# Kernel optimization log

Measured on AMD Instinct MI355X. Metric: run time of the kernel, lower is better.

## Reference

```python
import jax, jax.numpy as jnp
import numpy as np

B, S, E, H = 2, 2048, 1024, 16
DH = E // H  # 64


def setup_inputs() -> dict:
    key = jax.random.key(0)
    ks = jax.random.split(key, 10)
    scale = 1.0 / np.sqrt(E)
    x = jax.random.normal(ks[0], (B, S, E), dtype=jnp.float32)
    mask = jax.random.randint(ks[1], (B, S), 0, 2, dtype=jnp.int32)
    # per-head Q/K/V projections stacked: [H, E, DH] (x @ W, torch Linear transposed)
    wq = jax.random.normal(ks[2], (H, E, DH), dtype=jnp.float32) * scale
    wk = jax.random.normal(ks[3], (H, E, DH), dtype=jnp.float32) * scale
    wv = jax.random.normal(ks[4], (H, E, DH), dtype=jnp.float32) * scale
    bq = jax.random.normal(ks[5], (H, DH), dtype=jnp.float32) * scale
    bk = jax.random.normal(ks[6], (H, DH), dtype=jnp.float32) * scale
    bv = jax.random.normal(ks[7], (H, DH), dtype=jnp.float32) * scale
    wo = jax.random.normal(ks[8], (E, E), dtype=jnp.float32) * scale
    bo = jax.random.normal(ks[9], (E,), dtype=jnp.float32) * scale
    return {"x": x, "mask": mask, "wq": wq, "bq": bq, "wk": wk, "bk": bk,
            "wv": wv, "bv": bv, "wo": wo, "bo": bo}


def reference(x, mask, wq, bq, wk, bk, wv, bv, wo, bo):
    # q,k,v: [B, H, S, DH]
    q = jnp.einsum('bse,hed->bhsd', x, wq) + bq[None, :, None, :]
    k = jnp.einsum('bse,hed->bhsd', x, wk) + bk[None, :, None, :]
    v = jnp.einsum('bse,hed->bhsd', x, wv) + bv[None, :, None, :]
    scores = jnp.einsum('bhsd,bhtd->bhst', q, k) / np.sqrt(DH)
    # padding mask on key axis: mask==0 -> -1e9 (as in masked_fill)
    scores = jnp.where(mask[:, None, None, :] == 0, jnp.float32(-1e9), scores)
    attn = jax.nn.softmax(scores, axis=-1)
    o = jnp.einsum('bhst,bhtd->bhsd', attn, v)
    # concat heads -> [B, S, E], then output projection
    o = o.transpose(0, 2, 1, 3).reshape(B, S, E)
    return o @ wo + bo
```

## Files before the change

### kernel.cpp

```cpp
#include <hip/hip_runtime.h>
#include <hip/hip_bf16.h>
#include <math.h>

#define Bsz 2
#define Ssz 2048
#define Esz 1024
#define Hsz 16
#define DHsz 64

typedef __bf16 bf16_t;
typedef __attribute__((ext_vector_type(8))) __bf16 bf16x8;
typedef __attribute__((ext_vector_type(4))) float f32x4;

typedef unsigned int u32;
typedef const __attribute__((address_space(1))) u32* gptr_t;
typedef __attribute__((address_space(3))) u32* lptr_t;

#if __has_builtin(__builtin_amdgcn_exp2f)
#define EXP2F(x) __builtin_amdgcn_exp2f(x)
#else
#define EXP2F(x) __expf((x)*0.69314718f)
#endif

__device__ __forceinline__ bf16_t to_bf16(float f) {
  union { float f; unsigned u; } v; v.f = f;
  unsigned r = (v.u + 0x7FFF + ((v.u >> 16) & 1)) >> 16;
  union { unsigned short s; bf16_t b; } o; o.s = (unsigned short)r;
  return o.b;
}

__device__ __forceinline__ unsigned pack2(float a, float b) {
  union { float f; unsigned u; } x, y; x.f = a; y.f = b;
  unsigned ra = (x.u + 0x7FFF + ((x.u >> 16) & 1)) >> 16;
  unsigned rb = (y.u + 0x7FFF + ((y.u >> 16) & 1)) >> 16;
  return ra | (rb << 16);
}

__device__ __forceinline__ f32x4 mfma16(bf16x8 a, bf16x8 b, f32x4 c) {
  return __builtin_amdgcn_mfma_f32_16x16x32_bf16(a, b, c, 0, 0, 0);
}

__device__ __forceinline__ void gload16(void* lds, const void* g) {
  __builtin_amdgcn_global_load_lds((gptr_t)g, (lptr_t)lds, 16, 0, 0);
}

__global__ void cast_x4(const float4* __restrict__ x, uint2* __restrict__ xb, int n4) {
  int i = blockIdx.x * blockDim.x + threadIdx.x;
  if (i < n4) {
    float4 v = x[i];
    uint2 o; o.x = pack2(v.x, v.y); o.y = pack2(v.z, v.w);
    xb[i] = o;
  }
}

__global__ void mask_f(const int* __restrict__ mask, float* __restrict__ mf, int n) {
  int i = blockIdx.x * blockDim.x + threadIdx.x;
  if (i < n) mf[i] = mask[i] ? 1.0f : 0.0f;
}

__global__ __launch_bounds__(256) void wtrans(
    const float* __restrict__ wq, const float* __restrict__ wk,
    const float* __restrict__ wv, const float* __restrict__ wo,
    bf16_t* __restrict__ wAll, bf16_t* __restrict__ wAllV, bf16_t* __restrict__ woT) {
  __shared__ bf16_t lT[64 * 72];
  const int et = blockIdx.x, h = blockIdx.y, z = blockIdx.z;
  const float* src; int srcLD; bf16_t* dst;
  if (z == 0)      { src = wq + ((size_t)h * Esz + et * 64) * DHsz; srcLD = DHsz; dst = wAll  + (size_t)(h * 64) * Esz; }
  else if (z == 1) { src = wk + ((size_t)h * Esz + et * 64) * DHsz; srcLD = DHsz; dst = wAll  + (size_t)(1024 + h * 64) * Esz; }
  else if (z == 2) { src = wv + ((size_t)h * Esz + et * 64) * DHsz; srcLD = DHsz; dst = wAllV + (size_t)(h * 64) * Esz; }
  else             { src = wo + (size_t)(et * 64) * Esz + h * 64;   srcLD = Esz;  dst = woT   + (size_t)(h * 64) * Esz; }
  const int t = threadIdx.x;
#pragma unroll
  for (int rr = 0; rr < 4; rr++) {
    int er = rr * 16 + (t >> 4);
    int dc = (t & 15) * 4;
    float4 v = *(const float4*)&src[(size_t)er * srcLD + dc];
    lT[(dc + 0) * 72 + er] = to_bf16(v.x);
    lT[(dc + 1) * 72 + er] = to_bf16(v.y);
    lT[(dc + 2) * 72 + er] = to_bf16(v.z);
    lT[(dc + 3) * 72 + er] = to_bf16(v.w);
  }
  __syncthreads();
#pragma unroll
  for (int rr = 0; rr < 2; rr++) {
    int d = rr * 32 + (t >> 3);
    int e8 = (t & 7) * 8;
    bf16x8 o = *(const bf16x8*)&lT[d * 72 + e8];
    *(bf16x8*)&dst[(size_t)d * Esz + et * 64 + e8] = o;
  }
}

template <int TM, int TN>
__device__ __forceinline__ void gemm_core(
    const bf16_t* __restrict__ Ab, const bf16_t* __restrict__ Bb, int K,
    bf16_t* lA, bf16_t* lB, f32x4 (&acc)[TM / 32][TN / 32]) {
  const int tid = threadIdx.x, lane = tid & 63, wvi = tid >> 6;
  const int g = lane >> 4, c = lane & 15, cw = c & 7;
  const int lrow = lane >> 3, sg = lane & 7;
  const int wm = wvi >> 1, wn = wvi & 1;
  for (int kc = 0; kc < K; kc += 64) {
#pragma unroll
    for (int j = 0; j < TM / 32; j++) {
      const int base = (j * 4 + wvi) * 8;
      const int row = base + lrow;
      gload16(lA + base * 64, Ab + (size_t)row * K + kc + ((sg ^ (row & 7)) * 8));
    }
#pragma unroll
    for (int j = 0; j < TN / 32; j++) {
      const int base = (j * 4 + wvi) * 8;
      const int row = base + lrow;
      gload16(lB + base * 64, Bb + (size_t)row * K + kc + ((sg ^ (row & 7)) * 8));
    }
    __syncthreads();
#pragma unroll
    for (int ksp = 0; ksp < 2; ksp++) {
      const int kg = (ksp * 4 + g) ^ cw;
      bf16x8 af[TM / 32], bfr[TN / 32];
#pragma unroll
      for (int mt = 0; mt < TM / 32; mt++)
        af[mt] = *(const bf16x8*)&lA[(wm * (TM / 2) + mt * 16 + c) * 64 + kg * 8];
#pragma unroll
      for (int nt = 0; nt < TN / 32; nt++)
        bfr[nt] = *(const bf16x8*)&lB[(wn * (TN / 2) + nt * 16 + c) * 64 + kg * 8];
#pragma unroll
      for (int mt = 0; mt < TM / 32; mt++)
#pragma unroll
        for (int nt = 0; nt < TN / 32; nt++)
          acc[mt][nt] = mfma16(af[mt], bfr[nt], acc[mt][nt]);
    }
    __syncthreads();
  }
}

__global__ __launch_bounds__(256, 2) void qk_gemm(
    const bf16_t* __restrict__ xb, const bf16_t* __restrict__ wAll,
    const float* __restrict__ bq, const float* __restrict__ bk,
    bf16_t* __restrict__ qb, bf16_t* __restrict__ kb) {
  __shared__ alignas(16) bf16_t lA[128 * 64];
  __shared__ alignas(16) bf16_t lB[128 * 64];
  f32x4 acc[4][4] = {};
  const int Mb = blockIdx.x * 128, Nb = blockIdx.y * 128;
  gemm_core<128, 128>(xb + (size_t)Mb * Esz, wAll + (size_t)Nb * Esz, Esz, lA, lB, acc);
  const int lane = threadIdx.x & 63, wvi = threadIdx.x >> 6;
  const int g = lane >> 4, c = lane & 15;
  const int wm = wvi >> 1, wn = wvi & 1;
#pragma unroll
  for (int nt = 0; nt < 4; nt++) {
    const int col = Nb + wn * 64 + nt * 16 + c;
    const int which = col >> 10, h = (col >> 6) & 15, d = col & 63;
    const float bias = (which ? bk : bq)[h * DHsz + d];
    const float scale = which ? 1.0f : 0.18033688011112042f;
    bf16_t* dst = which ? kb : qb;
#pragma unroll
    for (int mt = 0; mt < 4; mt++)
#pragma unroll
      for (int r = 0; r < 4; r++) {
        const int row = Mb + wm * 64 + mt * 16 + g * 4 + r;
        const int b = row >> 11, s = row & 2047;
        dst[(((size_t)(b * Hsz + h)) * Ssz + s) * DHsz + d] =
            to_bf16((acc[mt][nt][r] + bias) * scale);
      }
  }
}

__global__ __launch_bounds__(256, 2) void vt_gemm(
    const bf16_t* __restrict__ xb, const bf16_t* __restrict__ wAllV,
    const float* __restrict__ bv, bf16_t* __restrict__ vTb) {
  __shared__ alignas(16) bf16_t lA[64 * 64];
  __shared__ alignas(16) bf16_t lB[128 * 64];
  f32x4 acc[2][4] = {};
  const int Mb = blockIdx.x * 64, Nb = blockIdx.y * 128, b = blockIdx.z;
  gemm_core<64, 128>(wAllV + (size_t)Mb * Esz, xb + ((size_t)(b * Ssz) + Nb) * Esz,
                     Esz, lA, lB, acc);
  const int lane = threadIdx.x & 63, wvi = threadIdx.x >> 6;
  const int g = lane >> 4, c = lane & 15;
  const int wm = wvi >> 1, wn = wvi & 1;
#pragma unroll
  for (int mt = 0; mt < 2; mt++)
#pragma unroll
    for (int r = 0; r < 4; r++) {
      const int m = Mb + wm * 32 + mt * 16 + g * 4 + r;
      const float bias = bv[m];
      const size_t obase = ((size_t)(b * Hsz * DHsz + m)) * Ssz;
#pragma unroll
      for (int nt = 0; nt < 4; nt++) {
        const int s = Nb + wn * 64 + nt * 16 + c;
        vTb[obase + s] = to_bf16(acc[mt][nt][r] + bias);
      }
    }
}

__global__ __launch_bounds__(256, 3) void flash_attn(
    const bf16_t* __restrict__ qb, const bf16_t* __restrict__ kb,
    const bf16_t* __restrict__ vTb, const float* __restrict__ mf,
    bf16_t* __restrict__ Ob) {
  __shared__ alignas(16) bf16_t lK0[64 * 64];
  __shared__ alignas(16) bf16_t lV0[64 * 64];
  __shared__ alignas(16) bf16_t lK1[64 * 64];
  __shared__ alignas(16) bf16_t lV1[64 * 64];
  __shared__ alignas(16) bf16_t lP[4][32 * 64];
  __shared__ float lL[4][32];

  const int h = blockIdx.x, qt = blockIdx.y, b = blockIdx.z;
  const size_t bh = (size_t)(b * Hsz + h);
  const int tid = threadIdx.x, lane = tid & 63, wv = tid >> 6;
  const int g = lane >> 4, c = lane & 15, cw = c & 7;
  const int lrow = lane >> 3, sg = lane & 7;

  const bf16_t* Kbase = kb + bh * (size_t)Ssz * DHsz;
  const bf16_t* Vbase = vTb + bh * (size_t)DHsz * Ssz;
  const float* mbase = mf + b * Ssz;

  bf16x8 qf[2][2];
  const bf16_t* Qbase = qb + (bh * Ssz + qt * 128 + wv * 32) * DHsz;
#pragma unroll
  for (int qsub = 0; qsub < 2; qsub++)
#pragma unroll
    for (int ksp = 0; ksp < 2; ksp++)
      qf[qsub][ksp] = *(const bf16x8*)&Qbase[(qsub * 16 + c) * DHsz + ksp * 32 + g * 8];

  f32x4 o[2][4] = {};
  float lacc[2] = {0.f, 0.f};

  auto stage = [&](bf16_t* dK, bf16_t* dV, int tc) {
#pragma unroll
    for (int j = 0; j < 2; j++) {
      const int row = wv * 16 + j * 8 + lrow;
      const int kg = sg ^ (row & 7);
      gload16(dK + (wv * 16 + j * 8) * 64,
              Kbase + ((size_t)(tc * 64 + row)) * DHsz + kg * 8);
      gload16(dV + (wv * 16 + j * 8) * 64,
              Vbase + (size_t)row * Ssz + tc * 64 + kg * 8);
    }
  };

  auto compute = [&](const bf16_t* Kt, const bf16_t* Vt, int tc) {
    f32x4 st[2][4] = {};
#pragma unroll
    for (int ksp = 0; ksp < 2; ksp++) {
      const int kgr = (ksp * 4 + g) ^ cw;
#pragma unroll
      for (int nt = 0; nt < 4; nt++) {
        bf16x8 kf = *(const bf16x8*)&Kt[(nt * 16 + c) * 64 + kgr * 8];
        st[0][nt] = mfma16(kf, qf[0][ksp], st[0][nt]);
        st[1][nt] = mfma16(kf, qf[1][ksp], st[1][nt]);
      }
    }
    float4 mv[4];
#pragma unroll
    for (int nt = 0; nt < 4; nt++)
      mv[nt] = *(const float4*)&mbase[tc * 64 + nt * 16 + g * 4];
#pragma unroll
    for (int qsub = 0; qsub < 2; qsub++) {
      float part = 0.f;
#pragma unroll
      for (int nt = 0; nt < 4; nt++) {
        float p0 = EXP2F(st[qsub][nt][0]) * mv[nt].x;
        float p1 = EXP2F(st[qsub][nt][1]) * mv[nt].y;
        float p2 = EXP2F(st[qsub][nt][2]) * mv[nt].z;
        float p3 = EXP2F(st[qsub][nt][3]) * mv[nt].w;
        part += (p0 + p1) + (p2 + p3);
        const int pg = (nt * 2 + (g >> 1)) ^ cw;
        uint2 pv; pv.x = pack2(p0, p1); pv.y = pack2(p2, p3);
        *(uint2*)&lP[wv][(qsub * 16 + c) * 64 + pg * 8 + (g & 1) * 4] = pv;
      }
      lacc[qsub] += part;
    }
#pragma unroll
    for (int ksp = 0; ksp < 2; ksp++) {
      const int kgr = (ksp * 4 + g) ^ cw;
      bf16x8 pf0 = *(const bf16x8*)&lP[wv][(0 * 16 + c) * 64 + kgr * 8];
      bf16x8 pf1 = *(const bf16x8*)&lP[wv][(1 * 16 + c) * 64 + kgr * 8];
#pragma unroll
      for (int dt = 0; dt < 4; dt++) {
        bf16x8 vf = *(const bf16x8*)&Vt[(dt * 16 + c) * 64 + kgr * 8];
        o[0][dt] = mfma16(pf0, vf, o[0][dt]);
        o[1][dt] = mfma16(pf1, vf, o[1][dt]);
      }
    }
  };

  stage(lK0, lV0, 0);
  __syncthreads();
  for (int tc = 0; tc < 32; tc += 2) {
    stage(lK1, lV1, tc + 1);
    compute(lK0, lV0, tc);
    __syncthreads();
    if (tc + 2 < 32) stage(lK0, lV0, tc + 2);
    compute(lK1, lV1, tc + 1);
    __syncthreads();
  }

#pragma unroll
  for (int qsub = 0; qsub < 2; qsub++) {
    float v = lacc[qsub];
    v += __shfl_xor(v, 16);
    v += __shfl_xor(v, 32);
    lL[wv][qsub * 16 + c] = v;
  }
#pragma unroll
  for (int qsub = 0; qsub < 2; qsub++)
#pragma unroll
    for (int r = 0; r < 4; r++) {
      const int row = qsub * 16 + g * 4 + r;
      const float linv = 1.0f / fmaxf(lL[wv][row], 1e-30f);
      const size_t orow = (size_t)(b * Ssz + qt * 128 + wv * 32 + row) * Esz + h * DHsz;
#pragma unroll
      for (int dt = 0; dt < 4; dt++)
        Ob[orow + dt * 16 + c] = to_bf16(o[qsub][dt][r] * linv);
    }
}

__global__ __launch_bounds__(256, 2) void out_gemm(
    const bf16_t* __restrict__ Ob, const bf16_t* __restrict__ woT,
    const float* __restrict__ bo, float* __restrict__ out) {
  __shared__ alignas(16) bf16_t lA[128 * 64];
  __shared__ alignas(16) bf16_t lB[64 * 64];
  f32x4 acc[4][2] = {};
  const int Mb = blockIdx.x * 128, Nb = blockIdx.y * 64;
  gemm_core<128, 64>(Ob + (size_t)Mb * Esz, woT + (size_t)Nb * Esz, Esz, lA, lB, acc);
  const int lane = threadIdx.x & 63, wvi = threadIdx.x >> 6;
  const int g = lane >> 4, c = lane & 15;
  const int wm = wvi >> 1, wn = wvi & 1;
#pragma unroll
  for (int nt = 0; nt < 2; nt++) {
    const int col = Nb + wn * 32 + nt * 16 + c;
    const float bias = bo[col];
#pragma unroll
    for (int mt = 0; mt < 4; mt++)
#pragma unroll
      for (int r = 0; r < 4; r++) {
        const int row = Mb + wm * 64 + mt * 16 + g * 4 + r;
        out[(size_t)row * Esz + col] = acc[mt][nt][r] + bias;
      }
  }
}

extern "C" void kernel_launch(void* const* d_in, const int* in_sizes, int n_in,
                              void* d_out, int out_size, void* d_ws, size_t ws_size,
                              hipStream_t stream) {
  const float* x = (const float*)d_in[0];
  const int* mask = (const int*)d_in[1];
  const float* wq = (const float*)d_in[2];
  const float* bq = (const float*)d_in[3];
  const float* wk = (const float*)d_in[4];
  const float* bk = (const float*)d_in[5];
  const float* wv = (const float*)d_in[6];
  const float* bv = (const float*)d_in[7];
  const float* wo = (const float*)d_in[8];
  const float* bo = (const float*)d_in[9];
  float* out = (float*)d_out;

  char* ws = (char*)d_ws;
  size_t off = 0;
  auto take = [&](size_t bytes) -> char* {
    char* p = ws + off;
    off += (bytes + 255) & ~(size_t)255;
    return p;
  };
  bf16_t* xb    = (bf16_t*)take((size_t)Bsz * Ssz * Esz * 2);
  bf16_t* wAll  = (bf16_t*)take((size_t)2 * Esz * Esz * 2);
  bf16_t* wAllV = (bf16_t*)take((size_t)Esz * Esz * 2);
  bf16_t* woT   = (bf16_t*)take((size_t)Esz * Esz * 2);
  bf16_t* qb    = (bf16_t*)take((size_t)Bsz * Hsz * Ssz * DHsz * 2);
  bf16_t* kb    = (bf16_t*)take((size_t)Bsz * Hsz * Ssz * DHsz * 2);
  bf16_t* vTb   = (bf16_t*)take((size_t)Bsz * Hsz * Ssz * DHsz * 2);
  bf16_t* Ob    = (bf16_t*)take((size_t)Bsz * Ssz * Esz * 2);
  float*  mfp   = (float*)take((size_t)Bsz * Ssz * 4);

  const int n4 = Bsz * Ssz * Esz / 4;
  cast_x4<<<(n4 + 255) / 256, 256, 0, stream>>>((const float4*)x, (uint2*)xb, n4);
  mask_f<<<(Bsz * Ssz + 255) / 256, 256, 0, stream>>>(mask, mfp, Bsz * Ssz);
  wtrans<<<dim3(Esz / 64, Hsz, 4), 256, 0, stream>>>(wq, wk, wv, wo, wAll, wAllV, woT);

  qk_gemm<<<dim3(Bsz * Ssz / 128, 2 * Esz / 128), 256, 0, stream>>>(xb, wAll, bq, bk, qb, kb);
  vt_gemm<<<dim3(Esz / 64, Ssz / 128, Bsz), 256, 0, stream>>>(xb, wAllV, bv, vTb);
  flash_attn<<<dim3(Hsz, Ssz / 128, Bsz), 256, 0, stream>>>(qb, kb, vTb, mfp, Ob);
  out_gemm<<<dim3(Bsz * Ssz / 128, Esz / 64), 256, 0, stream>>>(Ob, woT, bo, out);
}
```

Baseline: 212.8 us.

## Fuse prep and QKV launches, fold mask into V, load K/V directly to registers

```diff
diff --git a/kernel.cpp b/kernel.cpp
--- a/kernel.cpp
+++ b/kernel.cpp
@@ -29,6 +29,14 @@
   return o.b;
 }
 
+__device__ __forceinline__ unsigned pack2_rtz(float a, float b) {
+#if __has_builtin(__builtin_amdgcn_perm)
+  return __builtin_amdgcn_perm(__float_as_uint(b), __float_as_uint(a), 0x07060302u);
+#else
+  return (__float_as_uint(a) >> 16) | (__float_as_uint(b) & 0xFFFF0000u);
+#endif
+}
+
 __device__ __forceinline__ unsigned pack2(float a, float b) {
   union { float f; unsigned u; } x, y; x.f = a; y.f = b;
   unsigned ra = (x.u + 0x7FFF + ((x.u >> 16) & 1)) >> 16;
@@ -44,49 +52,50 @@
   __builtin_amdgcn_global_load_lds((gptr_t)g, (lptr_t)lds, 16, 0, 0);
 }
 
-__global__ void cast_x4(const float4* __restrict__ x, uint2* __restrict__ xb, int n4) {
-  int i = blockIdx.x * blockDim.x + threadIdx.x;
-  if (i < n4) {
-    float4 v = x[i];
-    uint2 o; o.x = pack2(v.x, v.y); o.y = pack2(v.z, v.w);
-    xb[i] = o;
-  }
-}
-
-__global__ void mask_f(const int* __restrict__ mask, float* __restrict__ mf, int n) {
-  int i = blockIdx.x * blockDim.x + threadIdx.x;
-  if (i < n) mf[i] = mask[i] ? 1.0f : 0.0f;
-}
-
-__global__ __launch_bounds__(256) void wtrans(
+#define PREP_CAST 4096
+#define PREP_MASK 4112
+__global__ __launch_bounds__(256) void prep(
+    const float* __restrict__ x, const int* __restrict__ mask,
     const float* __restrict__ wq, const float* __restrict__ wk,
     const float* __restrict__ wv, const float* __restrict__ wo,
+    bf16_t* __restrict__ xb, bf16_t* __restrict__ mb,
     bf16_t* __restrict__ wAll, bf16_t* __restrict__ wAllV, bf16_t* __restrict__ woT) {
   __shared__ bf16_t lT[64 * 72];
-  const int et = blockIdx.x, h = blockIdx.y, z = blockIdx.z;
-  const float* src; int srcLD; bf16_t* dst;
-  if (z == 0)      { src = wq + ((size_t)h * Esz + et * 64) * DHsz; srcLD = DHsz; dst = wAll  + (size_t)(h * 64) * Esz; }
-  else if (z == 1) { src = wk + ((size_t)h * Esz + et * 64) * DHsz; srcLD = DHsz; dst = wAll  + (size_t)(1024 + h * 64) * Esz; }
-  else if (z == 2) { src = wv + ((size_t)h * Esz + et * 64) * DHsz; srcLD = DHsz; dst = wAllV + (size_t)(h * 64) * Esz; }
-  else             { src = wo + (size_t)(et * 64) * Esz + h * 64;   srcLD = Esz;  dst = woT   + (size_t)(h * 64) * Esz; }
-  const int t = threadIdx.x;
-#pragma unroll
-  for (int rr = 0; rr < 4; rr++) {
-    int er = rr * 16 + (t >> 4);
-    int dc = (t & 15) * 4;
-    float4 v = *(const float4*)&src[(size_t)er * srcLD + dc];
-    lT[(dc + 0) * 72 + er] = to_bf16(v.x);
-    lT[(dc + 1) * 72 + er] = to_bf16(v.y);
-    lT[(dc + 2) * 72 + er] = to_bf16(v.z);
-    lT[(dc + 3) * 72 + er] = to_bf16(v.w);
-  }
-  __syncthreads();
-#pragma unroll
-  for (int rr = 0; rr < 2; rr++) {
-    int d = rr * 32 + (t >> 3);
-    int e8 = (t & 7) * 8;
-    bf16x8 o = *(const bf16x8*)&lT[d * 72 + e8];
-    *(bf16x8*)&dst[(size_t)d * Esz + et * 64 + e8] = o;
+  const int bid = blockIdx.x, t = threadIdx.x;
+  if (bid < PREP_CAST) {
+    const int i = bid * 256 + t;
+    float4 v = ((const float4*)x)[i];
+    uint2 o; o.x = pack2(v.x, v.y); o.y = pack2(v.z, v.w);
+    ((uint2*)xb)[i] = o;
+  } else if (bid < PREP_MASK) {
+    const int i = (bid - PREP_CAST) * 256 + t;
+    mb[i] = to_bf16(mask[i] ? 1.0f : 0.0f);
+  } else {
+    const int t2 = bid - PREP_MASK;
+    const int et = t2 & 15, h = (t2 >> 4) & 15, z = t2 >> 8;
+    const float* src; int srcLD; bf16_t* dst;
+    if (z == 0)      { src = wq + ((size_t)h * Esz + et * 64) * DHsz; srcLD = DHsz; dst = wAll  + (size_t)(h * 64) * Esz; }
+    else if (z == 1) { src = wk + ((size_t)h * Esz + et * 64) * DHsz; srcLD = DHsz; dst = wAll  + (size_t)(1024 + h * 64) * Esz; }
+    else if (z == 2) { src = wv + ((size_t)h * Esz + et * 64) * DHsz; srcLD = DHsz; dst = wAllV + (size_t)(h * 64) * Esz; }
+    else             { src = wo + (size_t)(et * 64) * Esz + h * 64;   srcLD = Esz;  dst = woT   + (size_t)(h * 64) * Esz; }
+#pragma unroll
+    for (int rr = 0; rr < 4; rr++) {
+      int er = rr * 16 + (t >> 4);
+      int dc = (t & 15) * 4;
+      float4 v = *(const float4*)&src[(size_t)er * srcLD + dc];
+      lT[(dc + 0) * 72 + er] = to_bf16(v.x);
+      lT[(dc + 1) * 72 + er] = to_bf16(v.y);
+      lT[(dc + 2) * 72 + er] = to_bf16(v.z);
+      lT[(dc + 3) * 72 + er] = to_bf16(v.w);
+    }
+    __syncthreads();
+#pragma unroll
+    for (int rr = 0; rr < 2; rr++) {
+      int d = rr * 32 + (t >> 3);
+      int e8 = (t & 7) * 8;
+      bf16x8 o = *(const bf16x8*)&lT[d * 72 + e8];
+      *(bf16x8*)&dst[(size_t)d * Esz + et * 64 + e8] = o;
+    }
   }
 }
 
@@ -132,84 +141,75 @@
   }
 }
 
-__global__ __launch_bounds__(256, 2) void qk_gemm(
+__global__ __launch_bounds__(256, 2) void qkv_gemm(
     const bf16_t* __restrict__ xb, const bf16_t* __restrict__ wAll,
+    const bf16_t* __restrict__ wAllV, const bf16_t* __restrict__ mb,
     const float* __restrict__ bq, const float* __restrict__ bk,
-    bf16_t* __restrict__ qb, bf16_t* __restrict__ kb) {
+    const float* __restrict__ bv,
+    bf16_t* __restrict__ qb, bf16_t* __restrict__ kb, bf16_t* __restrict__ vTb) {
   __shared__ alignas(16) bf16_t lA[128 * 64];
   __shared__ alignas(16) bf16_t lB[128 * 64];
-  f32x4 acc[4][4] = {};
-  const int Mb = blockIdx.x * 128, Nb = blockIdx.y * 128;
-  gemm_core<128, 128>(xb + (size_t)Mb * Esz, wAll + (size_t)Nb * Esz, Esz, lA, lB, acc);
+  const int bid = blockIdx.x;
   const int lane = threadIdx.x & 63, wvi = threadIdx.x >> 6;
   const int g = lane >> 4, c = lane & 15;
   const int wm = wvi >> 1, wn = wvi & 1;
-#pragma unroll
-  for (int nt = 0; nt < 4; nt++) {
-    const int col = Nb + wn * 64 + nt * 16 + c;
-    const int which = col >> 10, h = (col >> 6) & 15, d = col & 63;
-    const float bias = (which ? bk : bq)[h * DHsz + d];
-    const float scale = which ? 1.0f : 0.18033688011112042f;
-    bf16_t* dst = which ? kb : qb;
-#pragma unroll
-    for (int mt = 0; mt < 4; mt++)
-#pragma unroll
-      for (int r = 0; r < 4; r++) {
-        const int row = Mb + wm * 64 + mt * 16 + g * 4 + r;
-        const int b = row >> 11, s = row & 2047;
-        dst[(((size_t)(b * Hsz + h)) * Ssz + s) * DHsz + d] =
-            to_bf16((acc[mt][nt][r] + bias) * scale);
-      }
-  }
-}
-
-__global__ __launch_bounds__(256, 2) void vt_gemm(
-    const bf16_t* __restrict__ xb, const bf16_t* __restrict__ wAllV,
-    const float* __restrict__ bv, bf16_t* __restrict__ vTb) {
-  __shared__ alignas(16) bf16_t lA[64 * 64];
-  __shared__ alignas(16) bf16_t lB[128 * 64];
-  f32x4 acc[2][4] = {};
-  const int Mb = blockIdx.x * 64, Nb = blockIdx.y * 128, b = blockIdx.z;
-  gemm_core<64, 128>(wAllV + (size_t)Mb * Esz, xb + ((size_t)(b * Ssz) + Nb) * Esz,
-                     Esz, lA, lB, acc);
-  const int lane = threadIdx.x & 63, wvi = threadIdx.x >> 6;
-  const int g = lane >> 4, c = lane & 15;
-  const int wm = wvi >> 1, wn = wvi & 1;
-#pragma unroll
-  for (int mt = 0; mt < 2; mt++)
-#pragma unroll
-    for (int r = 0; r < 4; r++) {
-      const int m = Mb + wm * 32 + mt * 16 + g * 4 + r;
-      const float bias = bv[m];
-      const size_t obase = ((size_t)(b * Hsz * DHsz + m)) * Ssz;
-#pragma unroll
-      for (int nt = 0; nt < 4; nt++) {
-        const int s = Nb + wn * 64 + nt * 16 + c;
-        vTb[obase + s] = to_bf16(acc[mt][nt][r] + bias);
-      }
-    }
-}
-
-__global__ __launch_bounds__(256, 3) void flash_attn(
+  if (bid < 512) {
+    f32x4 acc[4][4] = {};
+    const int Mb = (bid & 31) * 128, Nb = (bid >> 5) * 128;
+    gemm_core<128, 128>(xb + (size_t)Mb * Esz, wAll + (size_t)Nb * Esz, Esz, lA, lB, acc);
+#pragma unroll
+    for (int nt = 0; nt < 4; nt++) {
+      const int col = Nb + wn * 64 + nt * 16 + c;
+      const int which = col >> 10, h = (col >> 6) & 15, d = col & 63;
+      const float bias = (which ? bk : bq)[h * DHsz + d];
+      const float scale = which ? 1.0f : 0.18033688011112042f;
+      bf16_t* dst = which ? kb : qb;
+#pragma unroll
+      for (int mt = 0; mt < 4; mt++)
+#pragma unroll
+        for (int r = 0; r < 4; r++) {
+          const int row = Mb + wm * 64 + mt * 16 + g * 4 + r;
+          const int b = row >> 11, s = row & 2047;
+          dst[(((size_t)(b * Hsz + h)) * Ssz + s) * DHsz + d] =
+              to_bf16((acc[mt][nt][r] + bias) * scale);
+        }
+    }
+  } else {
+    const int t2 = bid - 512;
+    f32x4 acc[2][4] = {};
+    const int Mb = (t2 & 15) * 64, Nb = ((t2 >> 4) & 15) * 128, b = t2 >> 8;
+    gemm_core<64, 128>(wAllV + (size_t)Mb * Esz, xb + ((size_t)(b * Ssz) + Nb) * Esz,
+                       Esz, lA, lB, acc);
+#pragma unroll
+    for (int nt = 0; nt < 4; nt++) {
+      const int s = Nb + wn * 64 + nt * 16 + c;
+      const float mval = (float)mb[b * Ssz + s];
+#pragma unroll
+      for (int mt = 0; mt < 2; mt++)
+#pragma unroll
+        for (int r = 0; r < 4; r++) {
+          const int m = Mb + wm * 32 + mt * 16 + g * 4 + r;
+          const size_t obase = ((size_t)(b * Hsz * DHsz + m)) * Ssz;
+          vTb[obase + s] = to_bf16((acc[mt][nt][r] + bv[m]) * mval);
+        }
+    }
+  }
+}
+
+__global__ __launch_bounds__(256, 2) void flash_attn(
     const bf16_t* __restrict__ qb, const bf16_t* __restrict__ kb,
-    const bf16_t* __restrict__ vTb, const float* __restrict__ mf,
+    const bf16_t* __restrict__ vTb, const bf16_t* __restrict__ mb,
     bf16_t* __restrict__ Ob) {
-  __shared__ alignas(16) bf16_t lK0[64 * 64];
-  __shared__ alignas(16) bf16_t lV0[64 * 64];
-  __shared__ alignas(16) bf16_t lK1[64 * 64];
-  __shared__ alignas(16) bf16_t lV1[64 * 64];
   __shared__ alignas(16) bf16_t lP[4][32 * 64];
-  __shared__ float lL[4][32];
 
   const int h = blockIdx.x, qt = blockIdx.y, b = blockIdx.z;
   const size_t bh = (size_t)(b * Hsz + h);
   const int tid = threadIdx.x, lane = tid & 63, wv = tid >> 6;
   const int g = lane >> 4, c = lane & 15, cw = c & 7;
-  const int lrow = lane >> 3, sg = lane & 7;
-
-  const bf16_t* Kbase = kb + bh * (size_t)Ssz * DHsz;
-  const bf16_t* Vbase = vTb + bh * (size_t)DHsz * Ssz;
-  const float* mbase = mf + b * Ssz;
+
+  const bf16_t* Kbase = kb + bh * (size_t)Ssz * DHsz + c * DHsz + g * 8;
+  const bf16_t* Vbase = vTb + bh * (size_t)DHsz * Ssz + c * Ssz + g * 8;
+  const bf16_t* mbb = mb + b * Ssz + g * 8;
 
   bf16x8 qf[2][2];
   const bf16_t* Qbase = qb + (bh * Ssz + qt * 128 + wv * 32) * DHsz;
@@ -220,90 +220,76 @@
       qf[qsub][ksp] = *(const bf16x8*)&Qbase[(qsub * 16 + c) * DHsz + ksp * 32 + g * 8];
 
   f32x4 o[2][4] = {};
-  float lacc[2] = {0.f, 0.f};
-
-  auto stage = [&](bf16_t* dK, bf16_t* dV, int tc) {
-#pragma unroll
-    for (int j = 0; j < 2; j++) {
-      const int row = wv * 16 + j * 8 + lrow;
-      const int kg = sg ^ (row & 7);
-      gload16(dK + (wv * 16 + j * 8) * 64,
-              Kbase + ((size_t)(tc * 64 + row)) * DHsz + kg * 8);
-      gload16(dV + (wv * 16 + j * 8) * 64,
-              Vbase + (size_t)row * Ssz + tc * 64 + kg * 8);
-    }
+  f32x4 lac[2] = {};
+
+  auto loadK = [&](int tc, bf16x8 (&kf)[2][4]) {
+    const bf16_t* kp = Kbase + (size_t)tc * 64 * DHsz;
+#pragma unroll
+    for (int ksp = 0; ksp < 2; ksp++)
+#pragma unroll
+      for (int nt = 0; nt < 4; nt++)
+        kf[ksp][nt] = *(const bf16x8*)&kp[nt * 16 * DHsz + ksp * 32];
   };
 
-  auto compute = [&](const bf16_t* Kt, const bf16_t* Vt, int tc) {
+  auto body = [&](int tc, bf16x8 (&kcur)[2][4], bf16x8 (&knext)[2][4]) {
+    bf16x8 vf[2][4], mfr[2];
+    const bf16_t* vp = Vbase + tc * 64;
+#pragma unroll
+    for (int ksp = 0; ksp < 2; ksp++) {
+      mfr[ksp] = *(const bf16x8*)&mbb[tc * 64 + ksp * 32];
+#pragma unroll
+      for (int dt = 0; dt < 4; dt++)
+        vf[ksp][dt] = *(const bf16x8*)&vp[dt * 16 * Ssz + ksp * 32];
+    }
+    if (tc + 1 < 32) loadK(tc + 1, knext);
     f32x4 st[2][4] = {};
 #pragma unroll
-    for (int ksp = 0; ksp < 2; ksp++) {
-      const int kgr = (ksp * 4 + g) ^ cw;
+    for (int ksp = 0; ksp < 2; ksp++)
 #pragma unroll
       for (int nt = 0; nt < 4; nt++) {
-        bf16x8 kf = *(const bf16x8*)&Kt[(nt * 16 + c) * 64 + kgr * 8];
-        st[0][nt] = mfma16(kf, qf[0][ksp], st[0][nt]);
-        st[1][nt] = mfma16(kf, qf[1][ksp], st[1][nt]);
+        st[0][nt] = mfma16(kcur[ksp][nt], qf[0][ksp], st[0][nt]);
+        st[1][nt] = mfma16(kcur[ksp][nt], qf[1][ksp], st[1][nt]);
       }
-    }
-    float4 mv[4];
-#pragma unroll
-    for (int nt = 0; nt < 4; nt++)
-      mv[nt] = *(const float4*)&mbase[tc * 64 + nt * 16 + g * 4];
-#pragma unroll
-    for (int qsub = 0; qsub < 2; qsub++) {
-      float part = 0.f;
+#pragma unroll
+    for (int qsub = 0; qsub < 2; qsub++)
 #pragma unroll
       for (int nt = 0; nt < 4; nt++) {
-        float p0 = EXP2F(st[qsub][nt][0]) * mv[nt].x;
-        float p1 = EXP2F(st[qsub][nt][1]) * mv[nt].y;
-        float p2 = EXP2F(st[qsub][nt][2]) * mv[nt].z;
-        float p3 = EXP2F(st[qsub][nt][3]) * mv[nt].w;
-        part += (p0 + p1) + (p2 + p3);
+        float p0 = EXP2F(st[qsub][nt][0]);
+        float p1 = EXP2F(st[qsub][nt][1]);
+        float p2 = EXP2F(st[qsub][nt][2]);
+        float p3 = EXP2F(st[qsub][nt][3]);
         const int pg = (nt * 2 + (g >> 1)) ^ cw;
-        uint2 pv; pv.x = pack2(p0, p1); pv.y = pack2(p2, p3);
+        uint2 pv; pv.x = pack2_rtz(p0, p1); pv.y = pack2_rtz(p2, p3);
         *(uint2*)&lP[wv][(qsub * 16 + c) * 64 + pg * 8 + (g & 1) * 4] = pv;
       }
-      lacc[qsub] += part;
-    }
 #pragma unroll
     for (int ksp = 0; ksp < 2; ksp++) {
       const int kgr = (ksp * 4 + g) ^ cw;
       bf16x8 pf0 = *(const bf16x8*)&lP[wv][(0 * 16 + c) * 64 + kgr * 8];
       bf16x8 pf1 = *(const bf16x8*)&lP[wv][(1 * 16 + c) * 64 + kgr * 8];
+      lac[0] = mfma16(pf0, mfr[ksp], lac[0]);
+      lac[1] = mfma16(pf1, mfr[ksp], lac[1]);
 #pragma unroll
       for (int dt = 0; dt < 4; dt++) {
-        bf16x8 vf = *(const bf16x8*)&Vt[(dt * 16 + c) * 64 + kgr * 8];
-        o[0][dt] = mfma16(pf0, vf, o[0][dt]);
-        o[1][dt] = mfma16(pf1, vf, o[1][dt]);
+        o[0][dt] = mfma16(pf0, vf[ksp][dt], o[0][dt]);
+        o[1][dt] = mfma16(pf1, vf[ksp][dt], o[1][dt]);
       }
     }
   };
 
-  stage(lK0, lV0, 0);
-  __syncthreads();
+  bf16x8 kA[2][4], kB[2][4];
+  loadK(0, kA);
   for (int tc = 0; tc < 32; tc += 2) {
-    stage(lK1, lV1, tc + 1);
-    compute(lK0, lV0, tc);
-    __syncthreads();
-    if (tc + 2 < 32) stage(lK0, lV0, tc + 2);
-    compute(lK1, lV1, tc + 1);
-    __syncthreads();
-  }
-
-#pragma unroll
-  for (int qsub = 0; qsub < 2; qsub++) {
-    float v = lacc[qsub];
-    v += __shfl_xor(v, 16);
-    v += __shfl_xor(v, 32);
-    lL[wv][qsub * 16 + c] = v;
-  }
+    body(tc, kA, kB);
+    body(tc + 1, kB, kA);
+  }
+
 #pragma unroll
   for (int qsub = 0; qsub < 2; qsub++)
 #pragma unroll
     for (int r = 0; r < 4; r++) {
       const int row = qsub * 16 + g * 4 + r;
-      const float linv = 1.0f / fmaxf(lL[wv][row], 1e-30f);
+      const float linv = 1.0f / fmaxf(lac[qsub][r], 1e-30f);
       const size_t orow = (size_t)(b * Ssz + qt * 128 + wv * 32 + row) * Esz + h * DHsz;
 #pragma unroll
       for (int dt = 0; dt < 4; dt++)
@@ -366,15 +352,10 @@
   bf16_t* kb    = (bf16_t*)take((size_t)Bsz * Hsz * Ssz * DHsz * 2);
   bf16_t* vTb   = (bf16_t*)take((size_t)Bsz * Hsz * Ssz * DHsz * 2);
   bf16_t* Ob    = (bf16_t*)take((size_t)Bsz * Ssz * Esz * 2);
-  float*  mfp   = (float*)take((size_t)Bsz * Ssz * 4);
-
-  const int n4 = Bsz * Ssz * Esz / 4;
-  cast_x4<<<(n4 + 255) / 256, 256, 0, stream>>>((const float4*)x, (uint2*)xb, n4);
-  mask_f<<<(Bsz * Ssz + 255) / 256, 256, 0, stream>>>(mask, mfp, Bsz * Ssz);
-  wtrans<<<dim3(Esz / 64, Hsz, 4), 256, 0, stream>>>(wq, wk, wv, wo, wAll, wAllV, woT);
-
-  qk_gemm<<<dim3(Bsz * Ssz / 128, 2 * Esz / 128), 256, 0, stream>>>(xb, wAll, bq, bk, qb, kb);
-  vt_gemm<<<dim3(Esz / 64, Ssz / 128, Bsz), 256, 0, stream>>>(xb, wAllV, bv, vTb);
-  flash_attn<<<dim3(Hsz, Ssz / 128, Bsz), 256, 0, stream>>>(qb, kb, vTb, mfp, Ob);
+  bf16_t* mb    = (bf16_t*)take((size_t)Bsz * Ssz * 2);
+
+  prep<<<5136, 256, 0, stream>>>(x, mask, wq, wk, wv, wo, xb, mb, wAll, wAllV, woT);
+  qkv_gemm<<<1536, 256, 0, stream>>>(xb, wAll, wAllV, mb, bq, bk, bv, qb, kb, vTb);
+  flash_attn<<<dim3(Hsz, Ssz / 128, Bsz), 256, 0, stream>>>(qb, kb, vTb, mb, Ob);
   out_gemm<<<dim3(Bsz * Ssz / 128, Esz / 64), 256, 0, stream>>>(Ob, woT, bo, out);
 }
```

Result: slower. 271.3 us (+27.5%).
